# Performance work log

Hardware: AMD Instinct MI355X
Metric: run time of the kernel (lower is better)

The kernel has to match this reference:

```python
import jax, jax.numpy as jnp
import numpy as np

V = 96103   # pegasus-xsum vocab
D = 1024    # d_model
H = 16      # heads
DH = D // H
F = 4096    # ffn
L = 2       # enc and dec layers (reduced from 16 for the reference)
S = 512     # source length
T = 80      # max_length
B = 4       # batch of sources
NS = 5      # num_return_sequences
BN = B * NS # decode streams
TOPK = 100
EOS = 1
MINLEN = 7
EMB_SCALE = float(np.sqrt(D))


def ln(x):
    m = jnp.mean(x, -1, keepdims=True)
    v = jnp.mean((x - m) ** 2, -1, keepdims=True)
    return (x - m) * jax.lax.rsqrt(v + 1e-5)


def setup_inputs() -> dict:
    key = jax.random.key(0)
    ks = jax.random.split(key, 16)
    g = lambda k, s: (jax.random.normal(k, s) * 0.02).astype(jnp.float32)
    return {
        "ids": jax.random.randint(ks[0], (B, S), 0, 96000).astype(jnp.int32),
        "mask": jnp.ones((B, S), jnp.int32),
        "E": g(ks[1], (V, D)),
        "pos_e": g(ks[2], (S, D)),
        "pos_d": g(ks[3], (T, D)),
        "enc_attn_in": g(ks[4], (L, D, 3 * D)),
        "enc_attn_out": g(ks[5], (L, D, D)),
        "enc_ffn1": g(ks[6], (L, D, F)),
        "enc_ffn2": g(ks[7], (L, F, D)),
        "dec_sa_in": g(ks[8], (L, D, 3 * D)),
        "dec_sa_out": g(ks[9], (L, D, D)),
        "dec_ca_q": g(ks[10], (L, D, D)),
        "dec_ca_kv": g(ks[11], (L, D, 2 * D)),
        "dec_ca_out": g(ks[12], (L, D, D)),
        "dec_ffn1": g(ks[13], (L, D, F)),
        "dec_ffn2": g(ks[14], (L, F, D)),
    }


def _generate(ids, mask, E, pos_e, pos_d, enc_attn_in, enc_attn_out, enc_ffn1,
              enc_ffn2, dec_sa_in, dec_sa_out, dec_ca_q, dec_ca_kv, dec_ca_out,
              dec_ffn1, dec_ffn2):
    inv = 1.0 / float(np.sqrt(DH))
    # ---------------- encoder ----------------
    x = E[ids] * EMB_SCALE + pos_e[None]                       # [B,S,D]
    bias = (1.0 - mask.astype(jnp.float32))[:, None, None, :] * -1e9  # [B,1,1,S]
    for l in range(L):
        h = ln(x)
        qkv = h @ enc_attn_in[l]
        q = qkv[..., :D].reshape(B, S, H, DH)
        k = qkv[..., D:2 * D].reshape(B, S, H, DH)
        v = qkv[..., 2 * D:].reshape(B, S, H, DH)
        sc = jnp.einsum('bqhd,bkhd->bhqk', q, k) * inv + bias
        a = jnp.einsum('bhqk,bkhd->bqhd', jax.nn.softmax(sc, -1), v).reshape(B, S, D)
        x = x + a @ enc_attn_out[l]
        h = ln(x)
        x = x + jax.nn.gelu(h @ enc_ffn1[l]) @ enc_ffn2[l]
    enc = ln(x)
    # expand to BN = B * num_return_sequences decode streams
    enc_r = jnp.repeat(enc, NS, axis=0)                        # [BN,S,D]
    bias_r = jnp.repeat(bias, NS, axis=0)[:, :, 0, :]          # [BN,1,S]
    # precompute cross-attn K/V per decoder layer
    ckv = jnp.einsum('bsd,lde->lbse', enc_r, dec_ca_kv)        # [L,BN,S,2D]
    cK = ckv[..., :D].reshape(L, BN, S, H, DH)
    cV = ckv[..., D:].reshape(L, BN, S, H, DH)

    key_base = jax.random.key(1234)
    cache_k0 = jnp.zeros((L, BN, T, H, DH), jnp.float32)
    cache_v0 = jnp.zeros((L, BN, T, H, DH), jnp.float32)

    def step(carry, t):
        ck, cv, prev = carry
        x = E[prev] * EMB_SCALE + pos_d[t]                     # [BN,D]
        for l in range(L):
            h = ln(x)
            qkv = h @ dec_sa_in[l]
            q = qkv[:, :D].reshape(BN, H, DH)
            k = qkv[:, D:2 * D].reshape(BN, H, DH)
            v = qkv[:, 2 * D:].reshape(BN, H, DH)
            ck = ck.at[l, :, t].set(k)
            cv = cv.at[l, :, t].set(v)
            sc = jnp.einsum('bhd,bkhd->bhk', q, ck[l]) * inv
            sc = sc + jnp.where(jnp.arange(T) <= t, 0.0, -1e9)
            a = jnp.einsum('bhk,bkhd->bhd', jax.nn.softmax(sc, -1), cv[l]).reshape(BN, D)
            x = x + a @ dec_sa_out[l]
            h = ln(x)
            q2 = (h @ dec_ca_q[l]).reshape(BN, H, DH)
            sc2 = jnp.einsum('bhd,bshd->bhs', q2, cK[l]) * inv + bias_r
            a2 = jnp.einsum('bhs,bshd->bhd', jax.nn.softmax(sc2, -1), cV[l]).reshape(BN, D)
            x = x + a2 @ dec_ca_out[l]
            h = ln(x)
            x = x + jax.nn.gelu(h @ dec_ffn1[l]) @ dec_ffn2[l]
        x = ln(x)
        logits = x @ E.T                                       # [BN,V]
        forbid = (t < MINLEN - 1) & (jnp.arange(V) == EOS)     # min_length: block EOS
        logits = jnp.where(forbid, -1e9, logits)
        topv, topi = jax.lax.top_k(logits, TOPK)               # top_k=100 sampling
        sel = jax.random.categorical(jax.random.fold_in(key_base, t), topv)
        tok = jnp.take_along_axis(topi, sel[:, None], 1)[:, 0]
        lp = jnp.take_along_axis(jax.nn.log_softmax(logits, -1), tok[:, None], 1)[:, 0]
        return (ck, cv, tok), (tok, lp)

    init = (cache_k0, cache_v0, jnp.zeros((BN,), jnp.int32))  # start token = pad(0)
    _, (toks, lps) = jax.lax.scan(step, init, jnp.arange(T))
    return toks.T, lps.T                                       # [BN,T] each


def reference(ids, mask, E, pos_e, pos_d, enc_attn_in, enc_attn_out, enc_ffn1,
              enc_ffn2, dec_sa_in, dec_sa_out, dec_ca_q, dec_ca_kv, dec_ca_out,
              dec_ffn1, dec_ffn2):
    toks, _ = _generate(ids, mask, E, pos_e, pos_d, enc_attn_in, enc_attn_out,
                        enc_ffn1, enc_ffn2, dec_sa_in, dec_sa_out, dec_ca_q,
                        dec_ca_kv, dec_ca_out, dec_ffn1, dec_ffn2)
    # matches the torch module: [batch, num_seq, max_len] token ids
    return toks.reshape(B, NS, T)
```

## Files before the change

### kernel.cpp

```cpp
#include <hip/hip_runtime.h>
#include <cstdint>
#include <cstddef>

#define DEV __device__ __forceinline__

constexpr int V  = 96103;
constexpr int VPAD = 96104;
constexpr int D  = 1024;
constexpr int H  = 16;
constexpr int DH = 64;
constexpr int F  = 4096;
constexpr int NL = 2;
constexpr int S  = 512;
constexpr int T  = 80;
constexpr int B  = 4;
constexpr int NS = 5;
constexpr int BN = 20;
constexpr int KTOP = 100;
constexpr int EOS = 1;
constexpr int LCOLS = 188;
constexpr int LGRID = (V + LCOLS - 1) / LCOLS;


DEV float gelu_f(float x) {
  float x3 = x * x * x;
  float inner = 0.7978845608028654f * (x + 0.044715f * x3);
  float tt = tanhf(inner);
  return x * (0.5f * (1.0f + tt));
}

DEV void tf2x32(unsigned k0, unsigned k1, unsigned& x0, unsigned& x1) {
  unsigned ks2 = k0 ^ k1 ^ 0x1BD11BDAu;
#define TFR(rr) { x0 += x1; x1 = (x1 << rr) | (x1 >> (32 - rr)); x1 ^= x0; }
  x0 += k0; x1 += k1;
  TFR(13) TFR(15) TFR(26) TFR(6)
  x0 += k1;  x1 += ks2 + 1u;
  TFR(17) TFR(29) TFR(16) TFR(24)
  x0 += ks2; x1 += k0 + 2u;
  TFR(13) TFR(15) TFR(26) TFR(6)
  x0 += k0;  x1 += k1 + 3u;
  TFR(17) TFR(29) TFR(16) TFR(24)
  x0 += k1;  x1 += ks2 + 4u;
  TFR(13) TFR(15) TFR(26) TFR(6)
  x0 += ks2; x1 += k0 + 5u;
#undef TFR
}

DEV unsigned long long sort_key(float v, unsigned idx) {
  unsigned bb = __float_as_uint(v);
  bb = (bb & 0x80000000u) ? ~bb : (bb | 0x80000000u);
  return ((unsigned long long)bb << 32) | (unsigned long long)(0xFFFFFFFFu - idx);
}

template<int NWAVE>
DEV void ln_to_lds(const float* __restrict__ x, float* xs, int tid) {
  int w = tid >> 6, lane = tid & 63;
  for (int m = w; m < BN; m += NWAVE) {
    float4 v[4];
    float sum = 0.0f;
#pragma unroll
    for (int j = 0; j < 4; ++j) {
      v[j] = *(const float4*)(x + m * D + j * 256 + lane * 4);
      sum += v[j].x + v[j].y + v[j].z + v[j].w;
    }
#pragma unroll
    for (int o = 32; o > 0; o >>= 1) sum += __shfl_xor(sum, o);
    float mean = sum * (1.0f / 1024.0f);
    float vs = 0.0f;
#pragma unroll
    for (int j = 0; j < 4; ++j) {
      float a = v[j].x - mean, b = v[j].y - mean, c = v[j].z - mean, d = v[j].w - mean;
      vs += a * a + b * b + c * c + d * d;
    }
#pragma unroll
    for (int o = 32; o > 0; o >>= 1) vs += __shfl_xor(vs, o);
    float rsig = 1.0f / sqrtf(vs * (1.0f / 1024.0f) + 1e-5f);
#pragma unroll
    for (int j = 0; j < 4; ++j) {
      float4 ov;
      ov.x = (v[j].x - mean) * rsig; ov.y = (v[j].y - mean) * rsig;
      ov.z = (v[j].z - mean) * rsig; ov.w = (v[j].w - mean) * rsig;
      *(float4*)(xs + m * D + j * 256 + lane * 4) = ov;
    }
  }
}


__global__ __launch_bounds__(256) void embed_enc(const int* __restrict__ ids,
                                                 const float* __restrict__ E,
                                                 const float* __restrict__ pos_e,
                                                 float* __restrict__ xe) {
  int row = blockIdx.x;
  int id = ids[row];
  const float* er = E + (size_t)id * D;
  const float* pr = pos_e + (size_t)(row % S) * D;
  float* xr = xe + (size_t)row * D;
  for (int j = threadIdx.x; j < D; j += 256)
    xr[j] = er[j] * 32.0f + pr[j];
}

__global__ __launch_bounds__(256) void embed_dec(const float* __restrict__ E,
                                                 const float* __restrict__ pos_d,
                                                 const int* __restrict__ toks,
                                                 float* __restrict__ xd, int t) {
  int bn = blockIdx.x;
  int prev = (t == 0) ? 0 : toks[bn * T + (t - 1)];
  const float* er = E + (size_t)prev * D;
  const float* pr = pos_d + (size_t)t * D;
  float* xr = xd + (size_t)bn * D;
  for (int j = threadIdx.x; j < D; j += 256)
    xr[j] = er[j] * 32.0f + pr[j];
}


__global__ __launch_bounds__(256) void ln_kernel(const float* __restrict__ x,
                                                 float* __restrict__ y) {
  __shared__ float red[256];
  __shared__ float sv[2];
  int tid = threadIdx.x;
  const float* xr = x + (size_t)blockIdx.x * D;
  float4 v = *(const float4*)(xr + tid * 4);
  red[tid] = v.x + v.y + v.z + v.w;
  __syncthreads();
  for (int k = 128; k > 0; k >>= 1) { if (tid < k) red[tid] += red[tid + k]; __syncthreads(); }
  if (tid == 0) sv[0] = red[0] * (1.0f / 1024.0f);
  __syncthreads();
  float m = sv[0];
  float dx = v.x - m, dy = v.y - m, dz = v.z - m, dw = v.w - m;
  red[tid] = dx * dx + dy * dy + dz * dz + dw * dw;
  __syncthreads();
  for (int k = 128; k > 0; k >>= 1) { if (tid < k) red[tid] += red[tid + k]; __syncthreads(); }
  if (tid == 0) sv[1] = 1.0f / sqrtf(red[0] * (1.0f / 1024.0f) + 1e-5f);
  __syncthreads();
  float r = sv[1];
  float* yr = y + (size_t)blockIdx.x * D;
  float4 o; o.x = dx * r; o.y = dy * r; o.z = dz * r; o.w = dw * r;
  *(float4*)(yr + tid * 4) = o;
}


template<int EPI>
__global__ __launch_bounds__(256) void gemm128(const float* __restrict__ A,
                                               const float* __restrict__ W,
                                               const float* X, float* C,
                                               int Kd, int Nd) {
  __shared__ __align__(16) float As[8][128];
  __shared__ __align__(16) float Bs[8][128];
  int tid = threadIdx.x;
  int n0 = blockIdx.x * 128, m0 = blockIdx.y * 128;
  int tx = tid & 15, ty = tid >> 4;
  int ar = tid >> 1, ac = (tid & 1) * 4;
  int br = tid >> 5, bc = (tid & 31) * 4;
  float acc[8][8] = {};
  for (int k0 = 0; k0 < Kd; k0 += 8) {
    float4 av = *(const float4*)(A + (size_t)(m0 + ar) * Kd + k0 + ac);
    float4 wv = *(const float4*)(W + (size_t)(k0 + br) * Nd + n0 + bc);
    __syncthreads();
    As[ac + 0][ar] = av.x; As[ac + 1][ar] = av.y;
    As[ac + 2][ar] = av.z; As[ac + 3][ar] = av.w;
    *(float4*)&Bs[br][bc] = wv;
    __syncthreads();
#pragma unroll
    for (int k = 0; k < 8; ++k) {
      float a8[8], b8[8];
      *(float4*)&a8[0] = *(const float4*)&As[k][ty * 8];
      *(float4*)&a8[4] = *(const float4*)&As[k][ty * 8 + 4];
      *(float4*)&b8[0] = *(const float4*)&Bs[k][tx * 8];
      *(float4*)&b8[4] = *(const float4*)&Bs[k][tx * 8 + 4];
#pragma unroll
      for (int i = 0; i < 8; ++i)
#pragma unroll
        for (int j = 0; j < 8; ++j)
          acc[i][j] = fmaf(a8[i], b8[j], acc[i][j]);
    }
  }
#pragma unroll
  for (int i = 0; i < 8; ++i) {
    int m = m0 + ty * 8 + i;
#pragma unroll
    for (int j = 0; j < 8; ++j) {
      int n = n0 + tx * 8 + j;
      float r = acc[i][j];
      size_t off = (size_t)m * Nd + n;
      if (EPI == 1) r = X[off] + r;
      if (EPI == 2) r = gelu_f(r);
      C[off] = r;
    }
  }
}


__global__ __launch_bounds__(256) void enc_attn(const float* __restrict__ qkv,
                                                const int* __restrict__ mask,
                                                float* __restrict__ ab) {
  __shared__ __align__(16) float qv[64];
  __shared__ float sc[512];
  __shared__ float red[256];
  __shared__ float sv[2];
  int tid = threadIdx.x;
  int q = blockIdx.x % S;
  int h = (blockIdx.x / S) % H;
  int b = blockIdx.x / (S * H);
  const float* qrow = qkv + (size_t)(b * S + q) * (3 * D) + h * 64;
  if (tid < 64) qv[tid] = qrow[tid];
  __syncthreads();
  float lmax = -INFINITY;
  for (int k = tid; k < S; k += 256) {
    const float* kr = qkv + (size_t)(b * S + k) * (3 * D) + D + h * 64;
    float dot = 0.0f;
#pragma unroll
    for (int d4 = 0; d4 < 16; ++d4) {
      float4 kk = *(const float4*)(kr + d4 * 4);
      float4 qq = *(const float4*)(qv + d4 * 4);
      dot += qq.x * kk.x + qq.y * kk.y + qq.z * kk.z + qq.w * kk.w;
    }
    float bias = (1.0f - (float)mask[b * S + k]) * -1e9f;
    float val = dot * 0.125f + bias;
    sc[k] = val;
    lmax = fmaxf(lmax, val);
  }
  red[tid] = lmax; __syncthreads();
  for (int k = 128; k > 0; k >>= 1) { if (tid < k) red[tid] = fmaxf(red[tid], red[tid + k]); __syncthreads(); }
  if (tid == 0) sv[0] = red[0];
  __syncthreads();
  float mx = sv[0];
  float lsum = 0.0f;
  for (int k = tid; k < S; k += 256) { float e = expf(sc[k] - mx); sc[k] = e; lsum += e; }
  red[tid] = lsum; __syncthreads();
  for (int k = 128; k > 0; k >>= 1) { if (tid < k) red[tid] += red[tid + k]; __syncthreads(); }
  if (tid == 0) sv[1] = red[0];
  __syncthreads();
  float den = sv[1];
  for (int k = tid; k < S; k += 256) sc[k] = sc[k] / den;
  __syncthreads();
  int d = tid & 63, c = tid >> 6;
  const float* vb = qkv + (size_t)(b * S) * (3 * D) + 2 * D + h * 64 + d;
  float part = 0.0f;
  for (int k = c * 128; k < c * 128 + 128; ++k)
    part = fmaf(sc[k], vb[(size_t)k * (3 * D)], part);
  red[tid] = part; __syncthreads();
  if (tid < 64) {
    float o = red[tid] + red[tid + 64] + red[tid + 128] + red[tid + 192];
    ab[(size_t)(b * S + q) * D + h * 64 + tid] = o;
  }
}


template<int CT, int EPI, bool KV, bool LNIN>
__global__ __launch_bounds__(512) void dec_gemm(const float* __restrict__ x,
                                                const float* __restrict__ W,
                                                const float* Xres, float* Cout,
                                                float* __restrict__ cacheK,
                                                float* __restrict__ cacheV,
                                                int Kd, int Nd, int t, int l) {
  constexpr int KSP = 512 / CT;
  __shared__ float red[CT * 20 * (KSP + 1)];
  __shared__ float redw[CT * (KSP + 1)];
  __shared__ float sab[40];
  int tid = threadIdx.x;
  if constexpr (LNIN) {
    int w = tid >> 6, lane = tid & 63;
    for (int m = w; m < BN; m += 8) {
      const float* xr = x + (size_t)m * 1024 + lane * 16;
      float4 v[4];
      float sum = 0.0f;
#pragma unroll
      for (int j = 0; j < 4; ++j) {
        v[j] = *(const float4*)(xr + j * 4);
        sum += v[j].x + v[j].y + v[j].z + v[j].w;
      }
#pragma unroll
      for (int o = 32; o > 0; o >>= 1) sum += __shfl_xor(sum, o);
      float mean = sum * (1.0f / 1024.0f);
      float vs = 0.0f;
#pragma unroll
      for (int j = 0; j < 4; ++j) {
        float a = v[j].x - mean, b = v[j].y - mean, c2 = v[j].z - mean, d = v[j].w - mean;
        vs += a * a + b * b + c2 * c2 + d * d;
      }
#pragma unroll
      for (int o = 32; o > 0; o >>= 1) vs += __shfl_xor(vs, o);
      float rstd = 1.0f / sqrtf(vs * (1.0f / 1024.0f) + 1e-5f);
      if (lane == 0) { sab[m] = rstd; sab[20 + m] = -mean * rstd; }
    }
    __syncthreads();
  }
  int c = tid % CT, ks = tid / CT;
  int klen = Kd / KSP;
  const float* Wp = W + (size_t)(ks * klen) * Nd + blockIdx.x * CT + c;
  float acc[20] = {};
  float accw = 0.0f;
  for (int kk = 0; kk < klen; kk += 8) {
    float wv[8];
#pragma unroll
    for (int u = 0; u < 8; ++u) wv[u] = Wp[(size_t)u * Nd];
    Wp += (size_t)8 * Nd;
    if constexpr (LNIN)
      accw += wv[0] + wv[1] + wv[2] + wv[3] + wv[4] + wv[5] + wv[6] + wv[7];
    int kb = ks * klen + kk;
#pragma unroll
    for (int m = 0; m < 20; ++m) {
      float4 x0 = *(const float4*)(x + (size_t)m * Kd + kb);
      float4 x1 = *(const float4*)(x + (size_t)m * Kd + kb + 4);
      float a = acc[m];
      a = fmaf(x0.x, wv[0], a); a = fmaf(x0.y, wv[1], a);
      a = fmaf(x0.z, wv[2], a); a = fmaf(x0.w, wv[3], a);
      a = fmaf(x1.x, wv[4], a); a = fmaf(x1.y, wv[5], a);
      a = fmaf(x1.z, wv[6], a); a = fmaf(x1.w, wv[7], a);
      acc[m] = a;
    }
  }
#pragma unroll
  for (int m = 0; m < 20; ++m) red[(c * 20 + m) * (KSP + 1) + ks] = acc[m];
  if constexpr (LNIN) redw[c * (KSP + 1) + ks] = accw;
  __syncthreads();
  if (tid < CT * 20) {
    int cc = tid % CT, m = tid / CT;
    const float* rp = red + (cc * 20 + m) * (KSP + 1);
    float s = 0.0f;
#pragma unroll
    for (int k2 = 0; k2 < KSP; ++k2) s += rp[k2];
    if constexpr (LNIN) {
      const float* rw = redw + cc * (KSP + 1);
      float sw = 0.0f;
#pragma unroll
      for (int k2 = 0; k2 < KSP; ++k2) sw += rw[k2];
      s = sab[m] * s + sab[20 + m] * sw;
    }
    int ng = blockIdx.x * CT + cc;
    if constexpr (KV) {
      if (ng < D) {
        Cout[(size_t)m * Nd + ng] = s;
      } else if (ng < 2 * D) {
        cacheK[(((size_t)l * BN + m) * T + t) * D + (ng - D)] = s;
      } else {
        cacheV[(((size_t)l * BN + m) * T + t) * D + (ng - 2 * D)] = s;
      }
    } else {
      size_t off = (size_t)m * Nd + ng;
      if (EPI == 1) s = Xres[off] + s;
      if (EPI == 2) s = gelu_f(s);
      Cout[off] = s;
    }
  }
}


__global__ __launch_bounds__(128) void dec_self_attn(const float* __restrict__ qkvd,
                                                     const float* __restrict__ cacheK,
                                                     const float* __restrict__ cacheV,
                                                     float* __restrict__ ad, int t, int l) {
  __shared__ __align__(16) float qv[64];
  __shared__ float sc[96];
  __shared__ float sv[2];
  int tid = threadIdx.x;
  int bn = blockIdx.x >> 4;
  int h = blockIdx.x & 15;
  int n = t + 1;
  if (tid < 64) qv[tid] = qkvd[(size_t)bn * (3 * D) + h * 64 + tid];
  __syncthreads();
  if (tid < n) {
    const float* kr = cacheK + (((size_t)l * BN + bn) * T + tid) * D + h * 64;
    float dot = 0.0f;
#pragma unroll
    for (int d4 = 0; d4 < 16; ++d4) {
      float4 kk = *(const float4*)(kr + d4 * 4);
      float4 qq = *(const float4*)(qv + d4 * 4);
      dot += qq.x * kk.x + qq.y * kk.y + qq.z * kk.z + qq.w * kk.w;
    }
    sc[tid] = dot * 0.125f;
  }
  __syncthreads();
  if (tid == 0) {
    float mx = -INFINITY;
    for (int k = 0; k < n; ++k) mx = fmaxf(mx, sc[k]);
    sv[0] = mx;
  }
  __syncthreads();
  if (tid < n) sc[tid] = expf(sc[tid] - sv[0]);
  __syncthreads();
  if (tid == 0) {
    float s = 0.0f;
    for (int k = 0; k < n; ++k) s += sc[k];
    sv[1] = s;
  }
  __syncthreads();
  if (tid < n) sc[tid] = sc[tid] / sv[1];
  __syncthreads();
  if (tid < 64) {
    const float* vb = cacheV + ((size_t)l * BN + bn) * T * D + h * 64 + tid;
    float o = 0.0f;
    for (int k = 0; k < n; ++k) o = fmaf(sc[k], vb[(size_t)k * D], o);
    ad[(size_t)bn * D + h * 64 + tid] = o;
  }
}


__global__ __launch_bounds__(256) void dec_cross_attn(const float* __restrict__ q2,
                                                      const float* __restrict__ cKV,
                                                      const int* __restrict__ mask,
                                                      float* __restrict__ ad, int l) {
  __shared__ __align__(16) float qv[64];
  __shared__ float sc[512];
  __shared__ float red[256];
  __shared__ float sv[2];
  int tid = threadIdx.x;
  int bn = blockIdx.x >> 4;
  int h = blockIdx.x & 15;
  int b = bn / NS;
  const float* base = cKV + ((size_t)l * B + b) * S * (2 * D);
  if (tid < 64) qv[tid] = q2[(size_t)bn * D + h * 64 + tid];
  __syncthreads();
  float lmax = -INFINITY;
  for (int s = tid; s < S; s += 256) {
    const float* kr = base + (size_t)s * (2 * D) + h * 64;
    float dot = 0.0f;
#pragma unroll
    for (int d4 = 0; d4 < 16; ++d4) {
      float4 kk = *(const float4*)(kr + d4 * 4);
      float4 qq = *(const float4*)(qv + d4 * 4);
      dot += qq.x * kk.x + qq.y * kk.y + qq.z * kk.z + qq.w * kk.w;
    }
    float bias = (1.0f - (float)mask[b * S + s]) * -1e9f;
    float val = dot * 0.125f + bias;
    sc[s] = val;
    lmax = fmaxf(lmax, val);
  }
  red[tid] = lmax; __syncthreads();
  for (int k = 128; k > 0; k >>= 1) { if (tid < k) red[tid] = fmaxf(red[tid], red[tid + k]); __syncthreads(); }
  if (tid == 0) sv[0] = red[0];
  __syncthreads();
  float mx = sv[0];
  float lsum = 0.0f;
  for (int s = tid; s < S; s += 256) { float e = expf(sc[s] - mx); sc[s] = e; lsum += e; }
  red[tid] = lsum; __syncthreads();
  for (int k = 128; k > 0; k >>= 1) { if (tid < k) red[tid] += red[tid + k]; __syncthreads(); }
  if (tid == 0) sv[1] = red[0];
  __syncthreads();
  float den = sv[1];
  for (int s = tid; s < S; s += 256) sc[s] = sc[s] / den;
  __syncthreads();
  int d = tid & 63, c = tid >> 6;
  const float* vb = base + D + h * 64 + d;
  float part = 0.0f;
  for (int s = c * 128; s < c * 128 + 128; ++s)
    part = fmaf(sc[s], vb[(size_t)s * (2 * D)], part);
  red[tid] = part; __syncthreads();
  if (tid < 64) {
    float o = red[tid] + red[tid + 64] + red[tid + 128] + red[tid + 192];
    ad[(size_t)bn * D + h * 64 + tid] = o;
  }
}


__global__ __launch_bounds__(256) void logits3(const float* __restrict__ xd,
                                               const float* __restrict__ E,
                                               float* __restrict__ logits) {
  __shared__ float xs[20 * 1024];
  int tid = threadIdx.x;
  ln_to_lds<4>(xd, xs, tid);
  __syncthreads();
  int n = blockIdx.x * LCOLS + tid;
  if (tid < LCOLS && n < V) {
    const float* er = E + (size_t)n * D;
    float acc[20] = {};
    for (int k = 0; k < 1024; k += 8) {
      float4 e0 = *(const float4*)(er + k);
      float4 e1 = *(const float4*)(er + k + 4);
#pragma unroll
      for (int m = 0; m < 20; ++m) {
        const float* xb = xs + m * 1024 + k;
        float4 x0 = *(const float4*)(xb);
        float4 x1 = *(const float4*)(xb + 4);
        float a = acc[m];
        a = fmaf(x0.x, e0.x, a); a = fmaf(x0.y, e0.y, a);
        a = fmaf(x0.z, e0.z, a); a = fmaf(x0.w, e0.w, a);
        a = fmaf(x1.x, e1.x, a); a = fmaf(x1.y, e1.y, a);
        a = fmaf(x1.z, e1.z, a); a = fmaf(x1.w, e1.w, a);
        acc[m] = a;
      }
    }
#pragma unroll
    for (int m = 0; m < 20; ++m)
      logits[(size_t)m * VPAD + n] = acc[m];
  } else if (n == V) {
#pragma unroll
    for (int m = 0; m < 20; ++m)
      logits[(size_t)m * VPAD + V] = -1e30f;
  }
}


__global__ __launch_bounds__(256) void topk_sample(const float* __restrict__ logits,
                                                   int* __restrict__ toks,
                                                   const float* __restrict__ E,
                                                   const float* __restrict__ pos_d,
                                                   float* __restrict__ xd, int t) {
  __shared__ unsigned long long keys[2048];
  __shared__ float svals[128];
  __shared__ unsigned sidx[128];
  __shared__ int stok;
  int tid = threadIdx.x;
  int bn = blockIdx.x;
  const float* row = logits + (size_t)bn * VPAD;

  float tv[8]; unsigned ti[8];
#pragma unroll
  for (int j = 0; j < 8; ++j) { tv[j] = -INFINITY; ti[j] = 0xFFFFFFFFu; }

  for (int i4 = tid * 4; i4 < VPAD; i4 += 1024) {
    float4 v4 = *(const float4*)(row + i4);
    float vv[4] = {v4.x, v4.y, v4.z, v4.w};
#pragma unroll
    for (int j = 0; j < 4; ++j) {
      int i = i4 + j;
      float v = vv[j];
      if (t < 6 && i == EOS) v = -1e9f;
      if (v > tv[7]) {
        tv[7] = v; ti[7] = (unsigned)i;
#pragma unroll
        for (int jj = 7; jj > 0; --jj) {
          if (tv[jj] > tv[jj - 1]) {
            float a = tv[jj]; tv[jj] = tv[jj - 1]; tv[jj - 1] = a;
            unsigned bi = ti[jj]; ti[jj] = ti[jj - 1]; ti[jj - 1] = bi;
          }
        }
      }
    }
  }
#pragma unroll
  for (int j = 0; j < 8; ++j) keys[tid * 8 + j] = ~sort_key(tv[j], ti[j]);
  __syncthreads();

  for (int ksz = 2; ksz <= 2048; ksz <<= 1) {
    for (int jj = ksz >> 1; jj > 0; jj >>= 1) {
      for (int i = tid; i < 2048; i += 256) {
        int ixj = i ^ jj;
        if (ixj > i) {
          unsigned long long a = keys[i], b2 = keys[ixj];
          bool up = ((i & ksz) == 0);
          if ((a > b2) == up) { keys[i] = b2; keys[ixj] = a; }
        }
      }
      __syncthreads();
    }
  }

  if (tid < KTOP) {
    unsigned long long kk = ~keys[tid];
    unsigned sb = (unsigned)(kk >> 32);
    unsigned idx = 0xFFFFFFFFu - (unsigned)(kk & 0xFFFFFFFFull);
    unsigned fb = (sb & 0x80000000u) ? (sb ^ 0x80000000u) : ~sb;
    float v = __uint_as_float(fb);
    unsigned a0 = 0u, a1 = (unsigned)t;
    tf2x32(0u, 1234u, a0, a1);
    unsigned c0 = 0u, c1 = (unsigned)(bn * KTOP + tid);
    tf2x32(a0, a1, c0, c1);
    unsigned bits = c0 ^ c1;
    float f = __uint_as_float((bits >> 9) | 0x3f800000u) - 1.0f;
    float u = fmaxf(f, 1.17549435e-38f);
    float g = -logf(-logf(u));
    svals[tid] = v + g;
    sidx[tid] = idx;
  }
  __syncthreads();
  if (tid == 0) {
    int best = 0; float bv = svals[0];
    for (int j = 1; j < KTOP; ++j) { if (svals[j] > bv) { bv = svals[j]; best = j; } }
    int tok = (int)sidx[best];
    toks[bn * T + t] = tok;
    stok = tok;
  }
  __syncthreads();
  if (t + 1 < T) {
    int tok = stok;
    const float* er = E + (size_t)tok * D;
    const float* pr = pos_d + (size_t)(t + 1) * D;
    for (int j = tid; j < D; j += 256)
      xd[(size_t)bn * D + j] = er[j] * 32.0f + pr[j];
  }
}


extern "C" void kernel_launch(void* const* d_in, const int* in_sizes, int n_in,
                              void* d_out, int out_size, void* d_ws, size_t ws_size,
                              hipStream_t stream) {
  (void)in_sizes; (void)n_in; (void)out_size; (void)ws_size;

  const int*   ids   = (const int*)d_in[0];
  const int*   maskp = (const int*)d_in[1];
  const float* E     = (const float*)d_in[2];
  const float* pos_e = (const float*)d_in[3];
  const float* pos_d = (const float*)d_in[4];
  const float* eai   = (const float*)d_in[5];
  const float* eao   = (const float*)d_in[6];
  const float* ef1   = (const float*)d_in[7];
  const float* ef2   = (const float*)d_in[8];
  const float* dsi   = (const float*)d_in[9];
  const float* dso   = (const float*)d_in[10];
  const float* dcq   = (const float*)d_in[11];
  const float* dckv  = (const float*)d_in[12];
  const float* dco   = (const float*)d_in[13];
  const float* df1   = (const float*)d_in[14];
  const float* df2   = (const float*)d_in[15];

  float* ws = (float*)d_ws;
  size_t o = 0;
  auto alloc = [&](size_t n) { size_t r = o; o += (n + 63) & ~(size_t)63; return r; };
  float* cKV    = ws + alloc((size_t)NL * B * S * 2 * D);
  float* cacheK = ws + alloc((size_t)NL * BN * T * D);
  float* cacheV = ws + alloc((size_t)NL * BN * T * D);
  float* xe     = ws + alloc((size_t)B * S * D);
  float* he     = ws + alloc((size_t)B * S * D);
  float* qkvb   = ws + alloc((size_t)B * S * 3 * D);
  float* ab     = ws + alloc((size_t)B * S * D);
  float* ffb    = ws + alloc((size_t)B * S * F);
  float* xd      = qkvb;
  float* q2      = xd + BN * D;
  float* ad      = q2 + BN * D;
  float* qkvd    = ad + BN * D;
  float* ffd     = qkvd + BN * 3 * D;
  float* logitsb = ffd + BN * F;
  int* toks = (int*)d_out;

  embed_enc<<<B * S, 256, 0, stream>>>(ids, E, pos_e, xe);
  for (int l = 0; l < NL; ++l) {
    ln_kernel<<<B * S, 256, 0, stream>>>(xe, he);
    gemm128<0><<<dim3(3 * D / 128, B * S / 128), 256, 0, stream>>>(
        he, eai + (size_t)l * D * 3 * D, nullptr, qkvb, D, 3 * D);
    enc_attn<<<B * H * S, 256, 0, stream>>>(qkvb, maskp, ab);
    gemm128<1><<<dim3(D / 128, B * S / 128), 256, 0, stream>>>(
        ab, eao + (size_t)l * D * D, xe, xe, D, D);
    ln_kernel<<<B * S, 256, 0, stream>>>(xe, he);
    gemm128<2><<<dim3(F / 128, B * S / 128), 256, 0, stream>>>(
        he, ef1 + (size_t)l * D * F, nullptr, ffb, D, F);
    gemm128<1><<<dim3(D / 128, B * S / 128), 256, 0, stream>>>(
        ffb, ef2 + (size_t)l * F * D, xe, xe, F, D);
  }
  ln_kernel<<<B * S, 256, 0, stream>>>(xe, he);
  for (int l = 0; l < NL; ++l) {
    gemm128<0><<<dim3(2 * D / 128, B * S / 128), 256, 0, stream>>>(
        he, dckv + (size_t)l * D * 2 * D, nullptr,
        cKV + (size_t)l * B * S * 2 * D, D, 2 * D);
  }

  embed_dec<<<BN, 256, 0, stream>>>(E, pos_d, toks, xd, 0);
  for (int t = 0; t < T; ++t) {
    for (int l = 0; l < NL; ++l) {
      dec_gemm<16, 0, true, true><<<3 * D / 16, 512, 0, stream>>>(
          xd, dsi + (size_t)l * D * 3 * D, nullptr, qkvd, cacheK, cacheV,
          D, 3 * D, t, l);
      dec_self_attn<<<BN * H, 128, 0, stream>>>(qkvd, cacheK, cacheV, ad, t, l);
      dec_gemm<8, 1, false, false><<<D / 8, 512, 0, stream>>>(
          ad, dso + (size_t)l * D * D, xd, xd, nullptr, nullptr, D, D, 0, 0);
      dec_gemm<8, 0, false, true><<<D / 8, 512, 0, stream>>>(
          xd, dcq + (size_t)l * D * D, nullptr, q2, nullptr, nullptr, D, D, 0, 0);
      dec_cross_attn<<<BN * H, 256, 0, stream>>>(q2, cKV, maskp, ad, l);
      dec_gemm<8, 1, false, false><<<D / 8, 512, 0, stream>>>(
          ad, dco + (size_t)l * D * D, xd, xd, nullptr, nullptr, D, D, 0, 0);
      dec_gemm<16, 2, false, true><<<F / 16, 512, 0, stream>>>(
          xd, df1 + (size_t)l * D * F, nullptr, ffd, nullptr, nullptr, D, F, 0, 0);
      dec_gemm<8, 1, false, false><<<D / 8, 512, 0, stream>>>(
          ffd, df2 + (size_t)l * F * D, xd, xd, nullptr, nullptr, F, D, 0, 0);
    }
    logits3<<<LGRID, 256, 0, stream>>>(xd, E, logitsb);
    topk_sample<<<BN, 256, 0, stream>>>(logitsb, toks, E, pos_d, xd, t);
  }
}
```

Baseline: 57.94 ms.

## Fuse LN+QKV projection into self-attention and LN+Q projection into cross-attention

```diff
diff --git a/kernel.cpp b/kernel.cpp
--- a/kernel.cpp
+++ b/kernel.cpp
@@ -83,6 +83,27 @@
       *(float4*)(xs + m * D + j * 256 + lane * 4) = ov;
     }
   }
+}
+
+DEV void row_ln_stats(const float* __restrict__ xd, int bn, float* xrow,
+                      float* wred, float& rstd, float& bco, int tid) {
+  int w = tid >> 6, lane = tid & 63;
+  float4 v = *(const float4*)(xd + (size_t)bn * D + w * 256 + lane * 4);
+  *(float4*)(xrow + w * 256 + lane * 4) = v;
+  float s = v.x + v.y + v.z + v.w;
+#pragma unroll
+  for (int o = 32; o > 0; o >>= 1) s += __shfl_xor(s, o);
+  if (lane == 0) wred[w] = s;
+  __syncthreads();
+  float mean = (wred[0] + wred[1] + wred[2] + wred[3]) * (1.0f / 1024.0f);
+  float a = v.x - mean, b = v.y - mean, c = v.z - mean, d = v.w - mean;
+  float s2 = a * a + b * b + c * c + d * d;
+#pragma unroll
+  for (int o = 32; o > 0; o >>= 1) s2 += __shfl_xor(s2, o);
+  if (lane == 0) wred[4 + w] = s2;
+  __syncthreads();
+  rstd = 1.0f / sqrtf((wred[4] + wred[5] + wred[6] + wred[7]) * (1.0f / 1024.0f) + 1e-5f);
+  bco = -mean * rstd;
 }
 
 
@@ -346,20 +367,51 @@
 }
 
 
-__global__ __launch_bounds__(128) void dec_self_attn(const float* __restrict__ qkvd,
-                                                     const float* __restrict__ cacheK,
-                                                     const float* __restrict__ cacheV,
-                                                     float* __restrict__ ad, int t, int l) {
-  __shared__ __align__(16) float qv[64];
+__global__ __launch_bounds__(256) void qkv_selfattn(const float* __restrict__ xd,
+                                                    const float* __restrict__ Wqkv,
+                                                    float* __restrict__ cacheK,
+                                                    float* __restrict__ cacheV,
+                                                    float* __restrict__ ad,
+                                                    int t, int l) {
+  __shared__ __align__(16) float xrow[1024];
+  __shared__ __align__(16) float qv[64], kt[64], vt[64];
   __shared__ float sc[96];
+  __shared__ float wred[8];
   __shared__ float sv[2];
   int tid = threadIdx.x;
-  int bn = blockIdx.x >> 4;
-  int h = blockIdx.x & 15;
+  int h = blockIdx.x / BN, bn = blockIdx.x % BN;
+  float rstd, bco;
+  row_ln_stats(xd, bn, xrow, wred, rstd, bco, tid);
+  __syncthreads();
+  if (tid < 192) {
+    int part = tid >> 6;
+    int c = tid & 63;
+    const float* Wp = Wqkv + (size_t)part * D + (size_t)h * 64 + c;
+    float acc = 0.0f, accw = 0.0f;
+    for (int k = 0; k < 1024; k += 8) {
+      float wv[8];
+#pragma unroll
+      for (int u = 0; u < 8; ++u) wv[u] = Wp[(size_t)(k + u) * (3 * D)];
+#pragma unroll
+      for (int u = 0; u < 8; ++u) {
+        acc = fmaf(xrow[k + u], wv[u], acc);
+        accw += wv[u];
+      }
+    }
+    float val = rstd * acc + bco * accw;
+    if (part == 0) {
+      qv[c] = val;
+    } else if (part == 1) {
+      kt[c] = val;
+      cacheK[(((size_t)l * BN + bn) * T + t) * D + h * 64 + c] = val;
+    } else {
+      vt[c] = val;
+      cacheV[(((size_t)l * BN + bn) * T + t) * D + h * 64 + c] = val;
+    }
+  }
+  __syncthreads();
   int n = t + 1;
-  if (tid < 64) qv[tid] = qkvd[(size_t)bn * (3 * D) + h * 64 + tid];
-  __syncthreads();
-  if (tid < n) {
+  if (tid < t) {
     const float* kr = cacheK + (((size_t)l * BN + bn) * T + tid) * D + h * 64;
     float dot = 0.0f;
 #pragma unroll
@@ -369,6 +421,15 @@
       dot += qq.x * kk.x + qq.y * kk.y + qq.z * kk.z + qq.w * kk.w;
     }
     sc[tid] = dot * 0.125f;
+  } else if (tid == t) {
+    float dot = 0.0f;
+#pragma unroll
+    for (int d4 = 0; d4 < 16; ++d4) {
+      float4 kk = *(const float4*)(kt + d4 * 4);
+      float4 qq = *(const float4*)(qv + d4 * 4);
+      dot += qq.x * kk.x + qq.y * kk.y + qq.z * kk.z + qq.w * kk.w;
+    }
+    sc[t] = dot * 0.125f;
   }
   __syncthreads();
   if (tid == 0) {
@@ -390,27 +451,56 @@
   if (tid < 64) {
     const float* vb = cacheV + ((size_t)l * BN + bn) * T * D + h * 64 + tid;
     float o = 0.0f;
-    for (int k = 0; k < n; ++k) o = fmaf(sc[k], vb[(size_t)k * D], o);
+    for (int k = 0; k < t; ++k) o = fmaf(sc[k], vb[(size_t)k * D], o);
+    o = fmaf(sc[t], vt[tid], o);
     ad[(size_t)bn * D + h * 64 + tid] = o;
   }
 }
 
 
-__global__ __launch_bounds__(256) void dec_cross_attn(const float* __restrict__ q2,
-                                                      const float* __restrict__ cKV,
-                                                      const int* __restrict__ mask,
-                                                      float* __restrict__ ad, int l) {
+__global__ __launch_bounds__(256) void caq_crossattn(const float* __restrict__ xd,
+                                                     const float* __restrict__ Wcq,
+                                                     const float* __restrict__ cKVl,
+                                                     const int* __restrict__ mask,
+                                                     float* __restrict__ ad) {
+  __shared__ __align__(16) float xrow[1024];
   __shared__ __align__(16) float qv[64];
   __shared__ float sc[512];
   __shared__ float red[256];
+  __shared__ float qred[256], qredw[256];
+  __shared__ float wred[8];
   __shared__ float sv[2];
   int tid = threadIdx.x;
-  int bn = blockIdx.x >> 4;
-  int h = blockIdx.x & 15;
+  int h = blockIdx.x / BN, bn = blockIdx.x % BN;
   int b = bn / NS;
-  const float* base = cKV + ((size_t)l * B + b) * S * (2 * D);
-  if (tid < 64) qv[tid] = q2[(size_t)bn * D + h * 64 + tid];
-  __syncthreads();
+  float rstd, bco;
+  row_ln_stats(xd, bn, xrow, wred, rstd, bco, tid);
+  __syncthreads();
+  {
+    int c = tid & 63, ks = tid >> 6;
+    const float* Wp = Wcq + (size_t)(ks * 256) * D + (size_t)h * 64 + c;
+    float acc = 0.0f, accw = 0.0f;
+    for (int k = 0; k < 256; k += 8) {
+      float wv[8];
+#pragma unroll
+      for (int u = 0; u < 8; ++u) wv[u] = Wp[(size_t)(k + u) * D];
+#pragma unroll
+      for (int u = 0; u < 8; ++u) {
+        acc = fmaf(xrow[ks * 256 + k + u], wv[u], acc);
+        accw += wv[u];
+      }
+    }
+    qred[ks * 64 + c] = acc;
+    qredw[ks * 64 + c] = accw;
+  }
+  __syncthreads();
+  if (tid < 64) {
+    float a = qred[tid] + qred[64 + tid] + qred[128 + tid] + qred[192 + tid];
+    float aw = qredw[tid] + qredw[64 + tid] + qredw[128 + tid] + qredw[192 + tid];
+    qv[tid] = rstd * a + bco * aw;
+  }
+  __syncthreads();
+  const float* base = cKVl + (size_t)b * S * (2 * D);
   float lmax = -INFINITY;
   for (int s = tid; s < S; s += 256) {
     const float* kr = base + (size_t)s * (2 * D) + h * 64;
@@ -622,6 +712,7 @@
   float* ffd     = qkvd + BN * 3 * D;
   float* logitsb = ffd + BN * F;
   int* toks = (int*)d_out;
+  (void)q2; (void)qkvd;
 
   embed_enc<<<B * S, 256, 0, stream>>>(ids, E, pos_e, xe);
   for (int l = 0; l < NL; ++l) {
@@ -647,15 +738,12 @@
   embed_dec<<<BN, 256, 0, stream>>>(E, pos_d, toks, xd, 0);
   for (int t = 0; t < T; ++t) {
     for (int l = 0; l < NL; ++l) {
-      dec_gemm<16, 0, true, true><<<3 * D / 16, 512, 0, stream>>>(
-          xd, dsi + (size_t)l * D * 3 * D, nullptr, qkvd, cacheK, cacheV,
-          D, 3 * D, t, l);
-      dec_self_attn<<<BN * H, 128, 0, stream>>>(qkvd, cacheK, cacheV, ad, t, l);
+      qkv_selfattn<<<H * BN, 256, 0, stream>>>(
+          xd, dsi + (size_t)l * D * 3 * D, cacheK, cacheV, ad, t, l);
       dec_gemm<8, 1, false, false><<<D / 8, 512, 0, stream>>>(
           ad, dso + (size_t)l * D * D, xd, xd, nullptr, nullptr, D, D, 0, 0);
-      dec_gemm<8, 0, false, true><<<D / 8, 512, 0, stream>>>(
-          xd, dcq + (size_t)l * D * D, nullptr, q2, nullptr, nullptr, D, D, 0, 0);
-      dec_cross_attn<<<BN * H, 256, 0, stream>>>(q2, cKV, maskp, ad, l);
+      caq_crossattn<<<H * BN, 256, 0, stream>>>(
+          xd, dcq + (size_t)l * D * D, cKV + (size_t)l * B * S * 2 * D, maskp, ad);
       dec_gemm<8, 1, false, false><<<D / 8, 512, 0, stream>>>(
           ad, dco + (size_t)l * D * D, xd, xd, nullptr, nullptr, D, D, 0, 0);
       dec_gemm<16, 2, false, true><<<F / 16, 512, 0, stream>>>(
```

Result: faster. 54.64 ms (-5.7%).
